# Optimization experiments

Measured on AMD Instinct MI355X. Metric: run time of the kernel, lower is better.

## Reference

```python
import jax, jax.numpy as jnp
import numpy as np

N_NODES = 100000
N_EDGES = 1600000
VOCAB = 1000
D_IN = 64
D_H = 128
D_OUT = 1
NEG_SLOPE = 0.2  # PyG GATConv default leaky_relu slope


def setup_inputs() -> dict:
    key = jax.random.key(0)
    ks = jax.random.split(key, 13)
    s_in = 1.0 / np.sqrt(D_IN)
    s_h = 1.0 / np.sqrt(D_H)
    return {
        "x": jax.random.randint(ks[0], (N_NODES,), 0, VOCAB),
        "edge_index": jax.random.randint(ks[1], (2, N_EDGES), 0, N_NODES),
        "node_embeddings": jax.random.normal(ks[2], (VOCAB, D_IN)) * 0.1,
        "W1": jax.random.normal(ks[3], (D_IN, D_H)) * s_in,
        "a_src1": jax.random.normal(ks[4], (D_H,)) * s_h,
        "a_dst1": jax.random.normal(ks[5], (D_H,)) * s_h,
        "b1": jnp.zeros((D_H,)),
        "W2": jax.random.normal(ks[6], (D_H, D_H)) * s_h,
        "a_src2": jax.random.normal(ks[7], (D_H,)) * s_h,
        "a_dst2": jax.random.normal(ks[8], (D_H,)) * s_h,
        "b2": jnp.zeros((D_H,)),
        "W_fc": jax.random.normal(ks[9], (2 * D_H, D_OUT)) * (1.0 / np.sqrt(2 * D_H)),
        "b_fc": jnp.zeros((D_OUT,)),
    }


def segment_softmax(logits, seg, n):
    # numerically-stable softmax over edges grouped by destination node
    mx = jax.ops.segment_max(logits, seg, num_segments=n)
    e = jnp.exp(logits - mx[seg])
    s = jax.ops.segment_sum(e, seg, num_segments=n)
    return e / (s[seg] + 1e-16)


def gat_conv(h, src, dst, W, a_src, a_dst, b):
    # single-head GATConv (PyG defaults: heads=1, negative_slope=0.2, bias)
    h = h @ W                                   # [N, D]
    logit = (h @ a_src)[src] + (h @ a_dst)[dst]  # [E]
    logit = jax.nn.leaky_relu(logit, NEG_SLOPE)
    alpha = segment_softmax(logit, dst, N_NODES)
    out = jax.ops.segment_sum(alpha[:, None] * h[src], dst, num_segments=N_NODES)
    return out + b


def reference(x, edge_index, node_embeddings, W1, a_src1, a_dst1, b1,
              W2, a_src2, a_dst2, b2, W_fc, b_fc):
    h = node_embeddings[x]                      # [N, D_IN]
    src, dst = edge_index[0], edge_index[1]
    # PyG GATConv adds self-loops by default
    loop = jnp.arange(N_NODES)
    src_sl = jnp.concatenate([src, loop])
    dst_sl = jnp.concatenate([dst, loop])
    h = jax.nn.gelu(gat_conv(h, src_sl, dst_sl, W1, a_src1, a_dst1, b1), approximate=False)
    h = jax.nn.gelu(gat_conv(h, src_sl, dst_sl, W2, a_src2, a_dst2, b2), approximate=False)
    # per-edge prediction: concat endpoint features (original edges, no self-loops)
    pair = jnp.concatenate([h[src], h[dst]], axis=-1)   # [E, 2*D_H]
    out = jax.nn.gelu(pair @ W_fc + b_fc, approximate=False)
    return out.squeeze(1)                       # [E]
```

## Files before the change

### kernel.cpp

```cpp
#include <hip/hip_runtime.h>
#include <hip/hip_bf16.h>

#define N_NODES 100000
#define N_EDGES 1600000
#define N_ESL   1700000
#define VOCAB   1000
#define D_IN    64
#define D_H     128
#define NEG_SLOPE 0.2f

#define BSH   7
#define NB    782
#define CAP   3072
#define CHUNK 16384

#define CO_EMB   0
#define CO_W1    64000
#define CO_AS1   72192
#define CO_AD1   72320
#define CO_B1    72448
#define CO_W2    72576
#define CO_AS2   88960
#define CO_AD2   89088
#define CO_B2    89216
#define CO_WFC   89344
#define CO_BFC   89600
#define CO_TOTAL 89601

__device__ __forceinline__ float us2f(unsigned short h){ union{unsigned v; float f;} c; c.v = ((unsigned)h)<<16; return c.f; }
__device__ __forceinline__ float gelu_f(float v){ return 0.5f*v*(1.0f + erff(v*0.7071067811865475f)); }
__device__ __forceinline__ float4 ldf4(const float* p){ return *reinterpret_cast<const float4*>(p); }
__device__ __forceinline__ void stf4(float* p, float4 v){ *reinterpret_cast<float4*>(p) = v; }

__device__ __forceinline__ float wred_sum(float v){
  #pragma unroll
  for (int m=32;m;m>>=1) v += __shfl_xor(v,m,64);
  return v;
}

__global__ __launch_bounds__(64) void k_detect(const unsigned* __restrict__ w, int* __restrict__ flag){
  int t = threadIdx.x;
  float cnt = 0.f;
  #pragma unroll
  for (int i=0;i<2;++i){
    unsigned v = w[t + 64*i];
    unsigned e = (v >> 7) & 0xFFu;
    cnt += (e >= 110u && e <= 126u) ? 1.f : 0.f;
  }
  cnt = wred_sum(cnt);
  if (t==0) *flag = (cnt >= 64.f) ? 1 : 0;
}

__global__ void k_convert(const void* p0, const void* p1, const void* p2, const void* p3,
    const void* p4, const void* p5, const void* p6, const void* p7, const void* p8,
    const void* p9, const void* p10, const int* __restrict__ flag, float* __restrict__ c){
  int i = blockIdx.x*blockDim.x + threadIdx.x;
  if (i >= CO_TOTAL) return;
  const void* src; int off;
  if      (i < CO_W1 ){ src=p0;  off=i;          }
  else if (i < CO_AS1){ src=p1;  off=i-CO_W1;    }
  else if (i < CO_AD1){ src=p2;  off=i-CO_AS1;   }
  else if (i < CO_B1 ){ src=p3;  off=i-CO_AD1;   }
  else if (i < CO_W2 ){ src=p4;  off=i-CO_B1;    }
  else if (i < CO_AS2){ src=p5;  off=i-CO_W2;    }
  else if (i < CO_AD2){ src=p6;  off=i-CO_AS2;   }
  else if (i < CO_B2 ){ src=p7;  off=i-CO_AD2;   }
  else if (i < CO_WFC){ src=p8;  off=i-CO_B2;    }
  else if (i < CO_BFC){ src=p9;  off=i-CO_WFC;   }
  else               { src=p10; off=i-CO_BFC;   }
  float v = (*flag) ? us2f(((const unsigned short*)src)[off]) : ((const float*)src)[off];
  c[i] = v;
}

__global__ __launch_bounds__(256) void k_prevec(const float* __restrict__ cw,
    float* __restrict__ va2, float* __restrict__ vd2){
  int t = threadIdx.x;
  int r = t & 127;
  const float* vec = cw + ((t < 128) ? CO_AS2 : CO_AD2);
  float s = 0.f;
  for (int j=0;j<D_H;++j) s = fmaf(cw[CO_W2 + r*D_H + j], vec[j], s);
  if (t < 128) va2[r] = s; else vd2[r] = s;
}

__global__ __launch_bounds__(64) void k_table1(const float* __restrict__ cw,
    float* __restrict__ table1, float* __restrict__ as1, float* __restrict__ ad1){
  const float* emb = cw + CO_EMB;
  const float* W1  = cw + CO_W1;
  int v = blockIdx.x; int t = threadIdx.x;
  __shared__ float er[D_IN];
  er[t] = emb[v*D_IN + t];
  __syncthreads();
  int d0 = t, d1 = t + 64;
  float a0 = 0.f, a1 = 0.f;
  for (int k=0;k<D_IN;++k){
    float e = er[k];
    a0 = fmaf(e, W1[k*D_H+d0], a0);
    a1 = fmaf(e, W1[k*D_H+d1], a1);
  }
  table1[v*D_H+d0] = a0; table1[v*D_H+d1] = a1;
  float ps = a0*cw[CO_AS1+d0] + a1*cw[CO_AS1+d1];
  float pd = a0*cw[CO_AD1+d0] + a1*cw[CO_AD1+d1];
  ps = wred_sum(ps); pd = wred_sum(pd);
  if (t==0){ as1[v]=ps; ad1[v]=pd; }
}

__global__ void k_nodelog(const int* __restrict__ x, const float* __restrict__ as1,
    const float* __restrict__ ad1, float* __restrict__ sA1, float* __restrict__ dA1){
  int i = blockIdx.x*blockDim.x + threadIdx.x;
  if (i < N_NODES){ int xs = x[i]; sA1[i] = as1[xs]; dA1[i] = ad1[xs]; }
}

__global__ __launch_bounds__(256) void k_bin(const int* __restrict__ src,
    const int* __restrict__ dst, int* __restrict__ gcur, unsigned* __restrict__ ebuf){
  __shared__ int hist[NB];
  __shared__ int cur[NB];
  int tid = threadIdx.x;
  int base0 = blockIdx.x * CHUNK;
  int n = N_ESL - base0; if (n > CHUNK) n = CHUNK;
  for (int i=tid; i<NB; i+=256) hist[i] = 0;
  __syncthreads();
  for (int k=tid; k<n; k+=256){
    int e = base0 + k;
    int d = (e < N_EDGES) ? dst[e] : (e - N_EDGES);
    atomicAdd(&hist[d>>BSH], 1);
  }
  __syncthreads();
  for (int b=tid; b<NB; b+=256){
    int c = hist[b];
    cur[b] = c ? atomicAdd(&gcur[b], c) : 0;
  }
  __syncthreads();
  for (int k=tid; k<n; k+=256){
    int e = base0 + k;
    int s, d;
    if (e < N_EDGES){ s = src[e]; d = dst[e]; } else { s = d = e - N_EDGES; }
    int b = d >> BSH;
    int pos = atomicAdd(&cur[b], 1);
    if (pos < CAP) ebuf[(size_t)b*CAP + pos] = (unsigned)(((d & 127) << 17) | s);
  }
}

__global__ __launch_bounds__(1024) void k_bscan(const int* __restrict__ gcur, int* __restrict__ csrbase){
  int t = threadIdx.x, lane = t & 63, wid = t >> 6;
  int c = (t < NB) ? gcur[t] : 0;
  if (c > CAP) c = CAP;
  int v = c;
  #pragma unroll
  for (int m=1;m<64;m<<=1){ int u = __shfl_up(v,m,64); if (lane>=m) v += u; }
  __shared__ int wsum[16], woff[16];
  if (lane==63) wsum[wid] = v;
  __syncthreads();
  if (t==0){ int run=0; for (int w=0;w<16;++w){ woff[w]=run; run+=wsum[w]; } }
  __syncthreads();
  v += woff[wid];
  if (t < NB) csrbase[t] = v - c;
}

__global__ __launch_bounds__(256) void k_group(const unsigned* __restrict__ ebuf,
    const int* __restrict__ gcur, const int* __restrict__ csrbase,
    int* __restrict__ csr, int* __restrict__ rowoff, int* __restrict__ rowcnt){
  __shared__ unsigned stage[CAP];
  __shared__ int hist[128], lofs[128], cur[128];
  int b = blockIdx.x, tid = threadIdx.x;
  int n = gcur[b]; if (n > CAP) n = CAP;
  int nodeBase = b << BSH;
  int cbase = csrbase[b];
  if (tid < 128) hist[tid] = 0;
  __syncthreads();
  for (int k=tid; k<n; k+=256){
    unsigned p = ebuf[(size_t)b*CAP + k];
    stage[k] = p;
    atomicAdd(&hist[p >> 17], 1);
  }
  __syncthreads();
  if (tid == 0){ int run=0; for (int i=0;i<128;++i){ lofs[i]=run; run+=hist[i]; } }
  __syncthreads();
  if (tid < 128){
    int d = nodeBase + tid;
    if (d < N_NODES){ rowoff[d] = cbase + lofs[tid]; rowcnt[d] = hist[tid]; }
    cur[tid] = lofs[tid];
  }
  __syncthreads();
  for (int k=tid; k<n; k+=256){
    unsigned p = stage[k];
    int pos = atomicAdd(&cur[p >> 17], 1);
    csr[cbase + pos] = (int)(p & 0x1FFFFu);
  }
}

template<int MODE>
__global__ __launch_bounds__(256) void k_agg(const int* __restrict__ rowoff,
    const int* __restrict__ rowcnt, const int* __restrict__ csr_src, const int* __restrict__ x,
    const float* __restrict__ sa, const float* __restrict__ danode,
    const float* __restrict__ feat, const float* __restrict__ cw,
    const float* __restrict__ va2, const float* __restrict__ vd2,
    float* __restrict__ out_h, float* __restrict__ p_lo, float* __restrict__ p_hi){
  int lane = threadIdx.x & 63;
  int node = blockIdx.x*4 + (threadIdx.x >> 6);
  if (node >= N_NODES) return;
  int start = rowoff[node];
  int nj = rowcnt[node];
  int end = start + nj;
  float dA = danode[node];

  float mx, inv;
  float w_sav = 0.f; int rb_sav = 0;
  if (nj <= 64){
    int p = start + lane;
    bool act = p < end;
    int s = 0; float l = -1e30f;
    if (act){
      s = csr_src[p];
      l = sa[s] + dA; l = (l > 0.f) ? l : NEG_SLOPE*l;
      rb_sav = (MODE == 0 ? x[s] : s) * D_H;
    }
    float m = l, ss = act ? 1.0f : 0.0f;
    #pragma unroll
    for (int off=32; off; off>>=1){
      float mo = __shfl_xor(m, off, 64);
      float so = __shfl_xor(ss, off, 64);
      float mn = fmaxf(m, mo);
      ss = ss*expf(m-mn) + so*expf(mo-mn);
      m = mn;
    }
    mx = m; inv = 1.0f/(ss + 1e-16f);
    w_sav = act ? expf(l - mx)*inv : 0.f;
  } else {
    float m = -1e30f, ss = 0.f;
    for (int p = start + lane; p < end; p += 64){
      int s = csr_src[p];
      float l = sa[s] + dA; l = (l > 0.f) ? l : NEG_SLOPE*l;
      float mn = fmaxf(m, l);
      ss = ss*expf(m-mn) + expf(l-mn);
      m = mn;
    }
    #pragma unroll
    for (int off=32; off; off>>=1){
      float mo = __shfl_xor(m, off, 64);
      float so = __shfl_xor(ss, off, 64);
      float mn = fmaxf(m, mo);
      ss = ss*expf(m-mn) + so*expf(mo-mn);
      m = mn;
    }
    mx = m; inv = 1.0f/(ss + 1e-16f);
  }

  int c0 = (lane & 31)*4, half = lane >> 5;
  float a0=0.f, a1=0.f, a2=0.f, a3=0.f;
  for (int t0 = start; t0 < end; t0 += 64){
    float w; int rb;
    if (nj <= 64){ w = w_sav; rb = rb_sav; }
    else {
      int p = t0 + lane;
      w = 0.f; rb = 0;
      if (p < end){
        int s = csr_src[p];
        float l = sa[s] + dA; l = (l > 0.f) ? l : NEG_SLOPE*l;
        w = expf(l - mx)*inv;
        rb = (MODE == 0 ? x[s] : s) * D_H;
      }
    }
    int cnt = end - t0; if (cnt > 64) cnt = 64;
    int mid = (cnt + 1) >> 1;
    int lo = half ? mid : 0;
    int hi = half ? cnt : mid;
    for (int j = lo; j < hi; j += 4){
      int nh = hi - j;
      float w0 = __shfl(w,  j,   64), w1 = __shfl(w,  j+1, 64);
      float w2 = __shfl(w,  j+2, 64), w3 = __shfl(w,  j+3, 64);
      int   r0 = __shfl(rb, j,   64), r1 = __shfl(rb, j+1, 64);
      int   r2 = __shfl(rb, j+2, 64), r3 = __shfl(rb, j+3, 64);
      float4 f0 = make_float4(0.f,0.f,0.f,0.f), f1 = f0, f2 = f0, f3 = f0;
      f0 = ldf4(feat + r0 + c0);
      if (nh > 1) f1 = ldf4(feat + r1 + c0);
      if (nh > 2) f2 = ldf4(feat + r2 + c0);
      if (nh > 3) f3 = ldf4(feat + r3 + c0);
      a0 = fmaf(w0, f0.x, a0); a1 = fmaf(w0, f0.y, a1);
      a2 = fmaf(w0, f0.z, a2); a3 = fmaf(w0, f0.w, a3);
      a0 = fmaf(w1, f1.x, a0); a1 = fmaf(w1, f1.y, a1);
      a2 = fmaf(w1, f1.z, a2); a3 = fmaf(w1, f1.w, a3);
      a0 = fmaf(w2, f2.x, a0); a1 = fmaf(w2, f2.y, a1);
      a2 = fmaf(w2, f2.z, a2); a3 = fmaf(w2, f2.w, a3);
      a0 = fmaf(w3, f3.x, a0); a1 = fmaf(w3, f3.y, a1);
      a2 = fmaf(w3, f3.z, a2); a3 = fmaf(w3, f3.w, a3);
    }
  }
  a0 += __shfl_xor(a0,32,64); a1 += __shfl_xor(a1,32,64);
  a2 += __shfl_xor(a2,32,64); a3 += __shfl_xor(a3,32,64);

  if (MODE == 0){
    float o0 = gelu_f(a0 + cw[CO_B1+c0]);
    float o1 = gelu_f(a1 + cw[CO_B1+c0+1]);
    float o2 = gelu_f(a2 + cw[CO_B1+c0+2]);
    float o3 = gelu_f(a3 + cw[CO_B1+c0+3]);
    if (!half) stf4(out_h + (size_t)node*D_H + c0, make_float4(o0,o1,o2,o3));
    float pl = o0*va2[c0] + o1*va2[c0+1] + o2*va2[c0+2] + o3*va2[c0+3];
    float ph = o0*vd2[c0] + o1*vd2[c0+1] + o2*vd2[c0+2] + o3*vd2[c0+3];
    #pragma unroll
    for (int off=16; off; off>>=1){ pl += __shfl_xor(pl,off,64); ph += __shfl_xor(ph,off,64); }
    if (lane == 0){ p_lo[node] = pl; p_hi[node] = ph; }
  } else if (MODE == 1){
    if (!half) stf4(out_h + (size_t)node*D_H + c0, make_float4(a0,a1,a2,a3));
  } else {
    float o0 = gelu_f(a0 + cw[CO_B2+c0]);
    float o1 = gelu_f(a1 + cw[CO_B2+c0+1]);
    float o2 = gelu_f(a2 + cw[CO_B2+c0+2]);
    float o3 = gelu_f(a3 + cw[CO_B2+c0+3]);
    float pl = o0*cw[CO_WFC+c0]     + o1*cw[CO_WFC+c0+1]
             + o2*cw[CO_WFC+c0+2]   + o3*cw[CO_WFC+c0+3];
    float ph = o0*cw[CO_WFC+D_H+c0]   + o1*cw[CO_WFC+D_H+c0+1]
             + o2*cw[CO_WFC+D_H+c0+2] + o3*cw[CO_WFC+D_H+c0+3];
    #pragma unroll
    for (int off=16; off; off>>=1){ pl += __shfl_xor(pl,off,64); ph += __shfl_xor(ph,off,64); }
    if (lane == 0){ p_lo[node] = pl; p_hi[node] = ph; }
  }
}

__global__ __launch_bounds__(256) void k_post(const float* __restrict__ agg2,
    const float* __restrict__ cw, float* __restrict__ p_lo, float* __restrict__ p_hi){
  __shared__ float xr[64][D_H];
  __shared__ float W[64][D_H];
  const float* W2 = cw + CO_W2;
  int tid = threadIdx.x;
  int cg = tid & 31;
  int rg = tid >> 5;
  int base = blockIdx.x * 64;

  for (int i = tid; i < 64*D_H/4; i += 256){
    int row = i >> 5, c4 = (i & 31) * 4;
    int rr = base + row;
    float4 v = (rr < N_NODES) ? ldf4(agg2 + (size_t)rr*D_H + c4) : make_float4(0.f,0.f,0.f,0.f);
    stf4(&xr[row][c4], v);
  }

  float4 acc[8];
  #pragma unroll
  for (int rs=0; rs<8; ++rs) acc[rs] = make_float4(0.f,0.f,0.f,0.f);

  #pragma unroll
  for (int hk = 0; hk < 2; ++hk){
    __syncthreads();
    for (int i = tid; i < 64*D_H/4; i += 256){
      int k = i >> 5, c4 = (i & 31) * 4;
      stf4(&W[k][c4], ldf4(W2 + (size_t)(hk*64 + k)*D_H + c4));
    }
    __syncthreads();
    for (int k = 0; k < 64; ++k){
      float4 wv = ldf4(&W[k][cg*4]);
      int kk = hk*64 + k;
      #pragma unroll
      for (int rs = 0; rs < 8; ++rs){
        float xv = xr[rs*8 + rg][kk];
        acc[rs].x = fmaf(xv, wv.x, acc[rs].x);
        acc[rs].y = fmaf(xv, wv.y, acc[rs].y);
        acc[rs].z = fmaf(xv, wv.z, acc[rs].z);
        acc[rs].w = fmaf(xv, wv.w, acc[rs].w);
      }
    }
  }

  float4 b2v = ldf4(cw + CO_B2  + cg*4);
  float4 wlo = ldf4(cw + CO_WFC + cg*4);
  float4 whi = ldf4(cw + CO_WFC + D_H + cg*4);
  #pragma unroll
  for (int rs = 0; rs < 8; ++rs){
    int rr = base + rs*8 + rg;
    float o0 = gelu_f(acc[rs].x + b2v.x);
    float o1 = gelu_f(acc[rs].y + b2v.y);
    float o2 = gelu_f(acc[rs].z + b2v.z);
    float o3 = gelu_f(acc[rs].w + b2v.w);
    float pl = o0*wlo.x + o1*wlo.y + o2*wlo.z + o3*wlo.w;
    float ph = o0*whi.x + o1*whi.y + o2*whi.z + o3*whi.w;
    #pragma unroll
    for (int off=16; off; off>>=1){ pl += __shfl_xor(pl,off,64); ph += __shfl_xor(ph,off,64); }
    if (cg == 0 && rr < N_NODES){ p_lo[rr] = pl; p_hi[rr] = ph; }
  }
}

__global__ __launch_bounds__(256) void k_matmul2(float* __restrict__ hbuf, const float* __restrict__ cw){
  const float* W2 = cw + CO_W2;
  __shared__ float xr[16][D_H];
  int tid = threadIdx.x;
  int col = tid & 127, half = tid >> 7;
  int base = blockIdx.x * 64;
  for (int t0=0; t0<64; t0+=16){
    int r0 = base + t0;
    for (int i=tid; i<16*D_H; i+=256){
      int rr = r0 + (i>>7);
      xr[i>>7][i&127] = (rr < N_NODES) ? hbuf[(size_t)rr*D_H + (i&127)] : 0.f;
    }
    __syncthreads();
    float acc[8];
    #pragma unroll
    for (int r=0;r<8;++r) acc[r] = 0.f;
    int rb = half*8;
    for (int k=0;k<D_H;++k){
      float wv = W2[k*D_H + col];
      #pragma unroll
      for (int r=0;r<8;++r) acc[r] = fmaf(xr[rb+r][k], wv, acc[r]);
    }
    #pragma unroll
    for (int r=0;r<8;++r){
      int rr = r0 + rb + r;
      if (rr < N_NODES) hbuf[(size_t)rr*D_H + col] = acc[r];
    }
    __syncthreads();
  }
}

__global__ void k_final(const int* __restrict__ src, const int* __restrict__ dst,
    const float* __restrict__ p_lo, const float* __restrict__ p_hi,
    const float* __restrict__ cw, const int* __restrict__ flag, void* __restrict__ out){
  int q = blockIdx.x*blockDim.x + threadIdx.x;
  int e0 = q*4;
  if (e0 >= N_EDGES) return;
  float bfc = cw[CO_BFC];
  if (e0 + 4 <= N_EDGES){
    int4 s4 = *reinterpret_cast<const int4*>(src + e0);
    int4 d4 = *reinterpret_cast<const int4*>(dst + e0);
    float4 v;
    v.x = gelu_f(p_lo[s4.x] + p_hi[d4.x] + bfc);
    v.y = gelu_f(p_lo[s4.y] + p_hi[d4.y] + bfc);
    v.z = gelu_f(p_lo[s4.z] + p_hi[d4.z] + bfc);
    v.w = gelu_f(p_lo[s4.w] + p_hi[d4.w] + bfc);
    if (*flag){
      __hip_bfloat16* o = (__hip_bfloat16*)out + e0;
      o[0]=__float2bfloat16(v.x); o[1]=__float2bfloat16(v.y);
      o[2]=__float2bfloat16(v.z); o[3]=__float2bfloat16(v.w);
    } else {
      stf4((float*)out + e0, v);
    }
  } else {
    for (int e = e0; e < N_EDGES; ++e){
      float v = gelu_f(p_lo[src[e]] + p_hi[dst[e]] + bfc);
      if (*flag) ((__hip_bfloat16*)out)[e] = __float2bfloat16(v);
      else       ((float*)out)[e] = v;
    }
  }
}

extern "C" void kernel_launch(void* const* d_in, const int* in_sizes, int n_in,
                              void* d_out, int out_size, void* d_ws, size_t ws_size,
                              hipStream_t stream){
  (void)in_sizes; (void)n_in; (void)out_size;
  const int* x  = (const int*)d_in[0];
  const int* ei = (const int*)d_in[1];
  const int* src = ei;
  const int* dst = ei + N_EDGES;

  char* base = (char*)d_ws;
  size_t off = 0;
  auto A = [&](size_t bytes)->size_t{ size_t r = off; off = (off + bytes + 255) & ~(size_t)255; return r; };
  size_t o_flag   = A(4);
  size_t o_cw     = A((size_t)CO_TOTAL*4);
  size_t o_va2    = A(D_H*4);
  size_t o_vd2    = A(D_H*4);
  size_t o_table1 = A((size_t)VOCAB*D_H*4);
  size_t o_as1    = A(VOCAB*4);
  size_t o_ad1    = A(VOCAB*4);
  size_t o_sA1    = A((size_t)N_NODES*4);
  size_t o_dA1    = A((size_t)N_NODES*4);
  size_t o_sA2    = A((size_t)N_NODES*4);
  size_t o_dA2    = A((size_t)N_NODES*4);
  size_t o_rowoff = A((size_t)N_NODES*4);
  size_t o_rowcnt = A((size_t)N_NODES*4);
  size_t o_plo    = A((size_t)N_NODES*4);
  size_t o_phi    = A((size_t)N_NODES*4);
  size_t o_gcur   = A((size_t)NB*4);
  size_t o_cbase  = A((size_t)NB*4);
  size_t o_csr    = A((size_t)N_ESL*4);
  size_t o_big    = A((size_t)N_NODES*D_H*4);
  size_t need_b   = off;
  size_t o_agg2   = A((size_t)N_NODES*D_H*4);
  size_t need_a   = off;

  int*   flag   = (int*)(base + o_flag);
  float* cw     = (float*)(base + o_cw);
  float* va2    = (float*)(base + o_va2);
  float* vd2    = (float*)(base + o_vd2);
  float* table1 = (float*)(base + o_table1);
  float* as1    = (float*)(base + o_as1);
  float* ad1    = (float*)(base + o_ad1);
  float* sA1    = (float*)(base + o_sA1);
  float* dA1    = (float*)(base + o_dA1);
  float* sA2    = (float*)(base + o_sA2);
  float* dA2    = (float*)(base + o_dA2);
  int*   rowoff = (int*)(base + o_rowoff);
  int*   rowcnt = (int*)(base + o_rowcnt);
  float* plo    = (float*)(base + o_plo);
  float* phi    = (float*)(base + o_phi);
  int*   gcur   = (int*)(base + o_gcur);
  int*   cbase  = (int*)(base + o_cbase);
  int*   csr    = (int*)(base + o_csr);
  float* hbuf   = (float*)(base + o_big);
  unsigned* ebuf= (unsigned*)(base + o_big);
  float* agg2   = (float*)(base + o_agg2);

  if (ws_size < need_b) return;
  bool patha = (ws_size >= need_a);

  k_detect<<<1, 64, 0, stream>>>((const unsigned*)d_in[2], flag);
  k_convert<<<(CO_TOTAL+255)/256, 256, 0, stream>>>(d_in[2], d_in[3], d_in[4], d_in[5],
      d_in[6], d_in[7], d_in[8], d_in[9], d_in[10], d_in[11], d_in[12], flag, cw);
  k_prevec<<<1, 256, 0, stream>>>(cw, va2, vd2);
  k_table1<<<VOCAB, 64, 0, stream>>>(cw, table1, as1, ad1);
  k_nodelog<<<(N_NODES+255)/256, 256, 0, stream>>>(x, as1, ad1, sA1, dA1);

  hipMemsetAsync(gcur, 0, (size_t)NB*4, stream);
  k_bin<<<(N_ESL+CHUNK-1)/CHUNK, 256, 0, stream>>>(src, dst, gcur, ebuf);
  k_bscan<<<1, 1024, 0, stream>>>(gcur, cbase);
  k_group<<<NB, 256, 0, stream>>>(ebuf, gcur, cbase, csr, rowoff, rowcnt);

  int nagg = (N_NODES+3)/4;
  k_agg<0><<<nagg, 256, 0, stream>>>(rowoff, rowcnt, csr, x, sA1, dA1, table1, cw, va2, vd2, hbuf, sA2, dA2);
  if (patha){
    k_agg<1><<<nagg, 256, 0, stream>>>(rowoff, rowcnt, csr, x, sA2, dA2, hbuf, cw, va2, vd2, agg2, nullptr, nullptr);
    k_post<<<(N_NODES+63)/64, 256, 0, stream>>>(agg2, cw, plo, phi);
  } else {
    k_matmul2<<<(N_NODES+63)/64, 256, 0, stream>>>(hbuf, cw);
    k_agg<2><<<nagg, 256, 0, stream>>>(rowoff, rowcnt, csr, x, sA2, dA2, hbuf, cw, va2, vd2, nullptr, plo, phi);
  }
  k_final<<<(N_EDGES/4+255)/256, 256, 0, stream>>>(src, dst, plo, phi, cw, flag, d_out);
}
```

Measured before the change: 382.0 us.

## Merge prevec into setup, vectorize binning loads, warp-scan grouping, unroll aggregation by 8

Merges the W2-attention prevector computation into the weight-conversion kernel as an extra block, which removes one launch. Edge binning and grouping now read int4/uint4 vectors, and the serial 128-entry prefix scan in k_group becomes a wavefront shuffle scan. The aggregation inner loop is unrolled to 8 neighbours, putting more feature loads in flight at the cost of more registers. The vectorized loads assume 16-byte alignment and chunk sizes that are multiples of 4, and block 351 depends on CO_TOTAL fitting into 351 blocks.

```diff
diff --git a/kernel.cpp b/kernel.cpp
--- a/kernel.cpp
+++ b/kernel.cpp
@@ -51,10 +51,29 @@
   if (t==0) *flag = (cnt >= 64.f) ? 1 : 0;
 }
 
-__global__ void k_convert(const void* p0, const void* p1, const void* p2, const void* p3,
+__global__ __launch_bounds__(256) void k_setup(const void* p0, const void* p1, const void* p2, const void* p3,
     const void* p4, const void* p5, const void* p6, const void* p7, const void* p8,
-    const void* p9, const void* p10, const int* __restrict__ flag, float* __restrict__ c){
-  int i = blockIdx.x*blockDim.x + threadIdx.x;
+    const void* p9, const void* p10, const int* __restrict__ flag, float* __restrict__ c,
+    float* __restrict__ va2, float* __restrict__ vd2){
+  int b = blockIdx.x;
+  if (b == 351){
+    int t = threadIdx.x;
+    int r = t & 127;
+    int f = *flag;
+    const float* w2f = (const float*)p5;
+    const unsigned short* w2h = (const unsigned short*)p5;
+    const float* af = (const float*)((t < 128) ? p6 : p7);
+    const unsigned short* ah = (const unsigned short*)((t < 128) ? p6 : p7);
+    float s = 0.f;
+    for (int j=0;j<D_H;++j){
+      float wv = f ? us2f(w2h[r*D_H+j]) : w2f[r*D_H+j];
+      float av = f ? us2f(ah[j]) : af[j];
+      s = fmaf(wv, av, s);
+    }
+    if (t < 128) va2[r] = s; else vd2[r] = s;
+    return;
+  }
+  int i = b*256 + threadIdx.x;
   if (i >= CO_TOTAL) return;
   const void* src; int off;
   if      (i < CO_W1 ){ src=p0;  off=i;          }
@@ -72,16 +91,6 @@
   c[i] = v;
 }
 
-__global__ __launch_bounds__(256) void k_prevec(const float* __restrict__ cw,
-    float* __restrict__ va2, float* __restrict__ vd2){
-  int t = threadIdx.x;
-  int r = t & 127;
-  const float* vec = cw + ((t < 128) ? CO_AS2 : CO_AD2);
-  float s = 0.f;
-  for (int j=0;j<D_H;++j) s = fmaf(cw[CO_W2 + r*D_H + j], vec[j], s);
-  if (t < 128) va2[r] = s; else vd2[r] = s;
-}
-
 __global__ __launch_bounds__(64) void k_table1(const float* __restrict__ cw,
     float* __restrict__ table1, float* __restrict__ as1, float* __restrict__ ad1){
   const float* emb = cw + CO_EMB;
@@ -119,10 +128,15 @@
   int n = N_ESL - base0; if (n > CHUNK) n = CHUNK;
   for (int i=tid; i<NB; i+=256) hist[i] = 0;
   __syncthreads();
-  for (int k=tid; k<n; k+=256){
+  for (int k = tid*4; k < n; k += 1024){
     int e = base0 + k;
-    int d = (e < N_EDGES) ? dst[e] : (e - N_EDGES);
-    atomicAdd(&hist[d>>BSH], 1);
+    int4 d4;
+    if (e + 4 <= N_EDGES) d4 = *reinterpret_cast<const int4*>(dst + e);
+    else d4 = make_int4(e-N_EDGES, e+1-N_EDGES, e+2-N_EDGES, e+3-N_EDGES);
+    atomicAdd(&hist[d4.x>>BSH], 1);
+    atomicAdd(&hist[d4.y>>BSH], 1);
+    atomicAdd(&hist[d4.z>>BSH], 1);
+    atomicAdd(&hist[d4.w>>BSH], 1);
   }
   __syncthreads();
   for (int b=tid; b<NB; b+=256){
@@ -130,13 +144,24 @@
     cur[b] = c ? atomicAdd(&gcur[b], c) : 0;
   }
   __syncthreads();
-  for (int k=tid; k<n; k+=256){
+  for (int k = tid*4; k < n; k += 1024){
     int e = base0 + k;
-    int s, d;
-    if (e < N_EDGES){ s = src[e]; d = dst[e]; } else { s = d = e - N_EDGES; }
-    int b = d >> BSH;
-    int pos = atomicAdd(&cur[b], 1);
-    if (pos < CAP) ebuf[(size_t)b*CAP + pos] = (unsigned)(((d & 127) << 17) | s);
+    int4 d4, s4;
+    if (e + 4 <= N_EDGES){
+      d4 = *reinterpret_cast<const int4*>(dst + e);
+      s4 = *reinterpret_cast<const int4*>(src + e);
+    } else {
+      d4 = make_int4(e-N_EDGES, e+1-N_EDGES, e+2-N_EDGES, e+3-N_EDGES);
+      s4 = d4;
+    }
+    int p0 = atomicAdd(&cur[d4.x>>BSH], 1);
+    if (p0 < CAP) ebuf[(size_t)(d4.x>>BSH)*CAP + p0] = (unsigned)(((d4.x & 127) << 17) | s4.x);
+    int p1 = atomicAdd(&cur[d4.y>>BSH], 1);
+    if (p1 < CAP) ebuf[(size_t)(d4.y>>BSH)*CAP + p1] = (unsigned)(((d4.y & 127) << 17) | s4.y);
+    int p2 = atomicAdd(&cur[d4.z>>BSH], 1);
+    if (p2 < CAP) ebuf[(size_t)(d4.z>>BSH)*CAP + p2] = (unsigned)(((d4.z & 127) << 17) | s4.z);
+    int p3 = atomicAdd(&cur[d4.w>>BSH], 1);
+    if (p3 < CAP) ebuf[(size_t)(d4.w>>BSH)*CAP + p3] = (unsigned)(((d4.w & 127) << 17) | s4.w);
   }
 }
 
@@ -160,25 +185,43 @@
     const int* __restrict__ gcur, const int* __restrict__ csrbase,
     int* __restrict__ csr, int* __restrict__ rowoff, int* __restrict__ rowcnt){
   __shared__ unsigned stage[CAP];
-  __shared__ int hist[128], lofs[128], cur[128];
+  __shared__ int hist[128], cur[128];
+  __shared__ int wtot;
   int b = blockIdx.x, tid = threadIdx.x;
   int n = gcur[b]; if (n > CAP) n = CAP;
   int nodeBase = b << BSH;
   int cbase = csrbase[b];
   if (tid < 128) hist[tid] = 0;
   __syncthreads();
-  for (int k=tid; k<n; k+=256){
+  int nv = n & ~3;
+  for (int k = tid*4; k < nv; k += 1024){
+    uint4 q = *reinterpret_cast<const uint4*>(ebuf + (size_t)b*CAP + k);
+    stage[k]   = q.x; atomicAdd(&hist[q.x >> 17], 1);
+    stage[k+1] = q.y; atomicAdd(&hist[q.y >> 17], 1);
+    stage[k+2] = q.z; atomicAdd(&hist[q.z >> 17], 1);
+    stage[k+3] = q.w; atomicAdd(&hist[q.w >> 17], 1);
+  }
+  for (int k = nv + tid; k < n; k += 256){
     unsigned p = ebuf[(size_t)b*CAP + k];
     stage[k] = p;
     atomicAdd(&hist[p >> 17], 1);
   }
   __syncthreads();
-  if (tid == 0){ int run=0; for (int i=0;i<128;++i){ lofs[i]=run; run+=hist[i]; } }
-  __syncthreads();
+  int v128 = 0;
   if (tid < 128){
+    int lane = tid & 63;
+    v128 = hist[tid];
+    #pragma unroll
+    for (int m=1;m<64;m<<=1){ int u = __shfl_up(v128,m,64); if (lane>=m) v128 += u; }
+    if (tid == 63) wtot = v128;
+  }
+  __syncthreads();
+  if (tid < 128){
+    int incl = v128 + ((tid >= 64) ? wtot : 0);
+    int excl = incl - hist[tid];
     int d = nodeBase + tid;
-    if (d < N_NODES){ rowoff[d] = cbase + lofs[tid]; rowcnt[d] = hist[tid]; }
-    cur[tid] = lofs[tid];
+    if (d < N_NODES){ rowoff[d] = cbase + excl; rowcnt[d] = hist[tid]; }
+    cur[tid] = excl;
   }
   __syncthreads();
   for (int k=tid; k<n; k+=256){
@@ -264,25 +307,26 @@
     int mid = (cnt + 1) >> 1;
     int lo = half ? mid : 0;
     int hi = half ? cnt : mid;
-    for (int j = lo; j < hi; j += 4){
-      int nh = hi - j;
-      float w0 = __shfl(w,  j,   64), w1 = __shfl(w,  j+1, 64);
-      float w2 = __shfl(w,  j+2, 64), w3 = __shfl(w,  j+3, 64);
-      int   r0 = __shfl(rb, j,   64), r1 = __shfl(rb, j+1, 64);
-      int   r2 = __shfl(rb, j+2, 64), r3 = __shfl(rb, j+3, 64);
-      float4 f0 = make_float4(0.f,0.f,0.f,0.f), f1 = f0, f2 = f0, f3 = f0;
-      f0 = ldf4(feat + r0 + c0);
-      if (nh > 1) f1 = ldf4(feat + r1 + c0);
-      if (nh > 2) f2 = ldf4(feat + r2 + c0);
-      if (nh > 3) f3 = ldf4(feat + r3 + c0);
-      a0 = fmaf(w0, f0.x, a0); a1 = fmaf(w0, f0.y, a1);
-      a2 = fmaf(w0, f0.z, a2); a3 = fmaf(w0, f0.w, a3);
-      a0 = fmaf(w1, f1.x, a0); a1 = fmaf(w1, f1.y, a1);
-      a2 = fmaf(w1, f1.z, a2); a3 = fmaf(w1, f1.w, a3);
-      a0 = fmaf(w2, f2.x, a0); a1 = fmaf(w2, f2.y, a1);
-      a2 = fmaf(w2, f2.z, a2); a3 = fmaf(w2, f2.w, a3);
-      a0 = fmaf(w3, f3.x, a0); a1 = fmaf(w3, f3.y, a1);
-      a2 = fmaf(w3, f3.z, a2); a3 = fmaf(w3, f3.w, a3);
+    for (int j = lo; j < hi; j += 8){
+      float wv[8]; int rv[8];
+      #pragma unroll
+      for (int u=0; u<8; ++u){
+        int idx = (j+u < hi) ? (j+u) : (hi-1);
+        wv[u] = __shfl(w,  idx, 64);
+        rv[u] = __shfl(rb, idx, 64);
+        if (j+u >= hi) wv[u] = 0.f;
+      }
+      float4 f[8];
+      #pragma unroll
+      for (int u=0; u<8; ++u){
+        f[u] = make_float4(0.f,0.f,0.f,0.f);
+        if (j+u < hi) f[u] = ldf4(feat + rv[u] + c0);
+      }
+      #pragma unroll
+      for (int u=0; u<8; ++u){
+        a0 = fmaf(wv[u], f[u].x, a0); a1 = fmaf(wv[u], f[u].y, a1);
+        a2 = fmaf(wv[u], f[u].z, a2); a3 = fmaf(wv[u], f[u].w, a3);
+      }
     }
   }
   a0 += __shfl_xor(a0,32,64); a1 += __shfl_xor(a1,32,64);
@@ -500,9 +544,8 @@
   bool patha = (ws_size >= need_a);
 
   k_detect<<<1, 64, 0, stream>>>((const unsigned*)d_in[2], flag);
-  k_convert<<<(CO_TOTAL+255)/256, 256, 0, stream>>>(d_in[2], d_in[3], d_in[4], d_in[5],
-      d_in[6], d_in[7], d_in[8], d_in[9], d_in[10], d_in[11], d_in[12], flag, cw);
-  k_prevec<<<1, 256, 0, stream>>>(cw, va2, vd2);
+  k_setup<<<352, 256, 0, stream>>>(d_in[2], d_in[3], d_in[4], d_in[5],
+      d_in[6], d_in[7], d_in[8], d_in[9], d_in[10], d_in[11], d_in[12], flag, cw, va2, vd2);
   k_table1<<<VOCAB, 64, 0, stream>>>(cw, table1, as1, ad1);
   k_nodelog<<<(N_NODES+255)/256, 256, 0, stream>>>(x, as1, ad1, sA1, dA1);
 
```

Result: no change. 389.3 us (+1.9%).
